# Performance work log

Measured on AMD Instinct MI355X. Metric: run time of the kernel, lower is better.

Reference implementation:

```python
import jax, jax.numpy as jnp
import numpy as np

FORWARD_STEPS = 50
DT = 0.1
EPS = 1e-5
BATCH = 1_000_000


def setup_inputs() -> dict:
    key = jax.random.key(0)
    k1, k2, k3 = jax.random.split(key, 3)
    # physically plausible ranges: speed 0-20 m/s, relative speed -2..2 m/s, gap 5-45 m
    vi = 20.0 * jax.random.uniform(k1, (BATCH,), dtype=jnp.float32)
    delta_v = 4.0 * jax.random.uniform(k2, (BATCH,), dtype=jnp.float32) - 2.0
    delta_d = 5.0 + 40.0 * jax.random.uniform(k3, (BATCH,), dtype=jnp.float32)
    # learned scalar IDM parameters (initializer values from the layer)
    params = {
        'vf': jnp.float32(25.0),
        'A': jnp.float32(2.0),
        'b': jnp.float32(3.0),
        's0': jnp.float32(3.0),
        'T': jnp.float32(2.0),
    }
    return {'vi': vi, 'delta_v': delta_v, 'delta_d': delta_d, **params}


def reference(vi, delta_v, delta_d, vf, A, b, s0, T):
    inv_2sqrtAb = 1.0 / (2.0 * jnp.sqrt(A * b))

    def step(carry, _):
        v, dv = carry
        s_star = s0 + jnp.maximum(0.0, v * T + v * dv * inv_2sqrtAb)
        ahat = A * (1.0 - (v / vf) ** 4 - (s_star / (delta_d + EPS)) ** 2)
        v = v + ahat * DT
        dv = dv - ahat * DT
        return (v, dv), ahat

    _, preds = jax.lax.scan(step, (vi, delta_v), None, length=FORWARD_STEPS)
    # preds: (steps, batch) -> (batch, steps) to match tf.stack(axis=1)
    return jnp.transpose(preds)
```

## Files before the change

kernel.cpp:

```cpp
#include <hip/hip_runtime.h>


namespace {

constexpr int STEPS = 50;
constexpr int BLOCK = 256;
constexpr float DT  = 0.1f;
constexpr float EPS = 1e-5f;

__global__ __launch_bounds__(BLOCK) void idm_forward(
    const float* __restrict__ vi_in,
    const float* __restrict__ dv_in,
    const float* __restrict__ dd_in,
    const float* __restrict__ p_vf,
    const float* __restrict__ p_A,
    const float* __restrict__ p_b,
    const float* __restrict__ p_s0,
    const float* __restrict__ p_T,
    float* __restrict__ out,
    int n)
{
    __shared__ __align__(16) float lds[BLOCK * STEPS];

    const int tid  = threadIdx.x;
    const int base = blockIdx.x * BLOCK;
    const int i    = base + tid;

    const float vf = p_vf[0];
    const float A  = p_A[0];
    const float b  = p_b[0];
    const float s0 = p_s0[0];
    const float T  = p_T[0];
    const float inv2   = 1.0f / (2.0f * sqrtf(A * b));
    const float inv_vf = 1.0f / vf;

    float v = 0.0f, dv = 0.0f, inv_dd = 1.0f;
    if (i < n) {
        v      = vi_in[i];
        dv     = dv_in[i];
        inv_dd = 1.0f / (dd_in[i] + EPS);
    }

    float acc[STEPS];
#pragma unroll
    for (int t = 0; t < STEPS; ++t) {
        const float s_star = s0 + fmaxf(0.0f, fmaf(v * dv, inv2, v * T));
        const float q  = s_star * inv_dd;
        const float r  = v * inv_vf;
        const float r2 = r * r;
        const float r4 = r2 * r2;
        const float ahat = A * (1.0f - r4 - q * q);
        acc[t] = ahat;
        v  = fmaf(ahat,  DT, v);
        dv = fmaf(ahat, -DT, dv);
    }

#pragma unroll
    for (int t = 0; t < STEPS; t += 2) {
        *reinterpret_cast<float2*>(&lds[tid * STEPS + t]) =
            make_float2(acc[t], acc[t + 1]);
    }
    __syncthreads();

    const long long out_base = (long long)base * STEPS;
    const long long total    = (long long)n * STEPS;
    int chunk = BLOCK * STEPS;
    if (out_base + chunk > total) chunk = (int)(total - out_base);

    float4* __restrict__ outv      = reinterpret_cast<float4*>(out + out_base);
    const float4* __restrict__ ldv = reinterpret_cast<const float4*>(lds);
    const int nv = chunk >> 2;
    for (int m = tid; m < nv; m += BLOCK) {
        outv[m] = ldv[m];
    }
    for (int k = (nv << 2) + tid; k < chunk; k += BLOCK) {
        out[out_base + k] = lds[k];
    }
}

}

extern "C" void kernel_launch(void* const* d_in, const int* in_sizes, int n_in,
                              void* d_out, int out_size, void* d_ws, size_t ws_size,
                              hipStream_t stream) {
    const float* vi = (const float*)d_in[0];
    const float* dv = (const float*)d_in[1];
    const float* dd = (const float*)d_in[2];
    const float* vf = (const float*)d_in[3];
    const float* A  = (const float*)d_in[4];
    const float* b  = (const float*)d_in[5];
    const float* s0 = (const float*)d_in[6];
    const float* T  = (const float*)d_in[7];
    float* out = (float*)d_out;

    const int n    = in_sizes[0];
    const int grid = (n + BLOCK - 1) / BLOCK;
    idm_forward<<<grid, BLOCK, 0, stream>>>(vi, dv, dd, vf, A, b, s0, T, out, n);
}
```

Before: 217.6 us.

## Stage output transpose per wavefront group through double-buffered LDS with nontemporal stores

Shrinks the LDS staging buffer from the whole block to two 64-thread group buffers. Groups are written and drained in turn, ping-ponging between the buffers, and the drain uses nontemporal float4 stores. The smaller LDS footprint and the occupancy hint of 6 blocks per CU are meant to let more blocks stay resident, which should help hide the store-bound output write. The cost is three extra block-wide barriers and serialized group drains, and the math also gains one fused multiply-add.

```diff
diff --git a/kernel.cpp b/kernel.cpp
--- a/kernel.cpp
+++ b/kernel.cpp
@@ -3,12 +3,17 @@
 
 namespace {
 
-constexpr int STEPS = 50;
-constexpr int BLOCK = 256;
+constexpr int STEPS   = 50;
+constexpr int BLOCK   = 256;
+constexpr int GROUP   = 64;
+constexpr int NGROUPS = BLOCK / GROUP;
 constexpr float DT  = 0.1f;
 constexpr float EPS = 1e-5f;
 
-__global__ __launch_bounds__(BLOCK) void idm_forward(
+typedef float f32x4 __attribute__((ext_vector_type(4)));
+typedef float f32x2 __attribute__((ext_vector_type(2)));
+
+__global__ __launch_bounds__(BLOCK, 6) void idm_forward(
     const float* __restrict__ vi_in,
     const float* __restrict__ dv_in,
     const float* __restrict__ dd_in,
@@ -20,7 +25,7 @@
     float* __restrict__ out,
     int n)
 {
-    __shared__ __align__(16) float lds[BLOCK * STEPS];
+    __shared__ __align__(16) float lds[2][GROUP * STEPS];
 
     const int tid  = threadIdx.x;
     const int base = blockIdx.x * BLOCK;
@@ -49,32 +54,54 @@
         const float r  = v * inv_vf;
         const float r2 = r * r;
         const float r4 = r2 * r2;
-        const float ahat = A * (1.0f - r4 - q * q);
+        const float ahat = A * fmaf(-q, q, 1.0f - r4);
         acc[t] = ahat;
         v  = fmaf(ahat,  DT, v);
         dv = fmaf(ahat, -DT, dv);
     }
 
+    const int g_of = tid >> 6;
+    const int l_of = tid & 63;
+
+    if (g_of == 0) {
 #pragma unroll
-    for (int t = 0; t < STEPS; t += 2) {
-        *reinterpret_cast<float2*>(&lds[tid * STEPS + t]) =
-            make_float2(acc[t], acc[t + 1]);
+        for (int t = 0; t < STEPS; t += 2) {
+            f32x2 w; w.x = acc[t]; w.y = acc[t + 1];
+            *reinterpret_cast<f32x2*>(&lds[0][l_of * STEPS + t]) = w;
+        }
     }
     __syncthreads();
 
-    const long long out_base = (long long)base * STEPS;
-    const long long total    = (long long)n * STEPS;
-    int chunk = BLOCK * STEPS;
-    if (out_base + chunk > total) chunk = (int)(total - out_base);
+    const long long total = (long long)n * STEPS;
 
-    float4* __restrict__ outv      = reinterpret_cast<float4*>(out + out_base);
-    const float4* __restrict__ ldv = reinterpret_cast<const float4*>(lds);
-    const int nv = chunk >> 2;
-    for (int m = tid; m < nv; m += BLOCK) {
-        outv[m] = ldv[m];
-    }
-    for (int k = (nv << 2) + tid; k < chunk; k += BLOCK) {
-        out[out_base + k] = lds[k];
+#pragma unroll
+    for (int g = 0; g < NGROUPS; ++g) {
+        if (g + 1 < NGROUPS && g_of == g + 1) {
+            const int nb = (g + 1) & 1;
+#pragma unroll
+            for (int t = 0; t < STEPS; t += 2) {
+                f32x2 w; w.x = acc[t]; w.y = acc[t + 1];
+                *reinterpret_cast<f32x2*>(&lds[nb][l_of * STEPS + t]) = w;
+            }
+        }
+
+        const long long gbase = (long long)(base + g * GROUP) * STEPS;
+        if (gbase < total) {
+            long long rem = total - gbase;
+            int chunk = GROUP * STEPS;
+            if (rem < chunk) chunk = (int)rem;
+            const int nv = chunk >> 2;
+            f32x4* __restrict__ outv      = reinterpret_cast<f32x4*>(out + gbase);
+            const f32x4* __restrict__ ldv =
+                reinterpret_cast<const f32x4*>(lds[g & 1]);
+            for (int m = tid; m < nv; m += BLOCK) {
+                __builtin_nontemporal_store(ldv[m], &outv[m]);
+            }
+            for (int k = (nv << 2) + tid; k < chunk; k += BLOCK) {
+                out[gbase + k] = lds[g & 1][k];
+            }
+        }
+        __syncthreads();
     }
 }
 
```

After: 228.0 us. +4.8%, slower.

## Stage output per wavefront in two half-waves to halve LDS and drop block barrier

Applied to the files above, without the earlier changes.

Output staging changes from one block-wide LDS buffer with a __syncthreads to a per-wavefront buffer holding 32 rows. Each half of the wave writes its 50 results in turn, and the whole wave then streams that half out with vector stores. LDS per block is halved, more blocks fit per CU (launch bounds now request 5), and the block barrier is gone, so the write-heavy kernel should overlap its stores better. It also folds the q*q term into an fma. Correctness depends on LDS ops within one wavefront staying in program order, since there is no barrier between reuse of the halves.

```diff
diff --git a/kernel.cpp b/kernel.cpp
--- a/kernel.cpp
+++ b/kernel.cpp
@@ -5,10 +5,14 @@
 
 constexpr int STEPS = 50;
 constexpr int BLOCK = 256;
+constexpr int HALF  = 32;
 constexpr float DT  = 0.1f;
 constexpr float EPS = 1e-5f;
 
-__global__ __launch_bounds__(BLOCK) void idm_forward(
+typedef float f32x4 __attribute__((ext_vector_type(4)));
+typedef float f32x2 __attribute__((ext_vector_type(2)));
+
+__global__ __launch_bounds__(BLOCK, 5) void idm_forward(
     const float* __restrict__ vi_in,
     const float* __restrict__ dv_in,
     const float* __restrict__ dd_in,
@@ -20,11 +24,12 @@
     float* __restrict__ out,
     int n)
 {
-    __shared__ __align__(16) float lds[BLOCK * STEPS];
+    __shared__ __align__(16) float lds[BLOCK / 64][HALF * STEPS];
 
     const int tid  = threadIdx.x;
-    const int base = blockIdx.x * BLOCK;
-    const int i    = base + tid;
+    const int wid  = tid >> 6;
+    const int lane = tid & 63;
+    const int i    = blockIdx.x * BLOCK + tid;
 
     const float vf = p_vf[0];
     const float A  = p_A[0];
@@ -49,32 +54,42 @@
         const float r  = v * inv_vf;
         const float r2 = r * r;
         const float r4 = r2 * r2;
-        const float ahat = A * (1.0f - r4 - q * q);
+        const float ahat = A * fmaf(-q, q, 1.0f - r4);
         acc[t] = ahat;
         v  = fmaf(ahat,  DT, v);
         dv = fmaf(ahat, -DT, dv);
     }
 
+    float* wbuf = lds[wid];
+    const long long total = (long long)n * STEPS;
+    const long long ebase = (long long)blockIdx.x * BLOCK + (wid << 6);
+
 #pragma unroll
-    for (int t = 0; t < STEPS; t += 2) {
-        *reinterpret_cast<float2*>(&lds[tid * STEPS + t]) =
-            make_float2(acc[t], acc[t + 1]);
-    }
-    __syncthreads();
+    for (int h = 0; h < 2; ++h) {
+        if ((lane >> 5) == h) {
+            const int l = lane & 31;
+#pragma unroll
+            for (int t = 0; t < STEPS; t += 2) {
+                f32x2 w; w.x = acc[t]; w.y = acc[t + 1];
+                *reinterpret_cast<f32x2*>(&wbuf[l * STEPS + t]) = w;
+            }
+        }
 
-    const long long out_base = (long long)base * STEPS;
-    const long long total    = (long long)n * STEPS;
-    int chunk = BLOCK * STEPS;
-    if (out_base + chunk > total) chunk = (int)(total - out_base);
-
-    float4* __restrict__ outv      = reinterpret_cast<float4*>(out + out_base);
-    const float4* __restrict__ ldv = reinterpret_cast<const float4*>(lds);
-    const int nv = chunk >> 2;
-    for (int m = tid; m < nv; m += BLOCK) {
-        outv[m] = ldv[m];
-    }
-    for (int k = (nv << 2) + tid; k < chunk; k += BLOCK) {
-        out[out_base + k] = lds[k];
+        const long long gbase = (ebase + h * HALF) * STEPS;
+        if (gbase < total) {
+            long long rem = total - gbase;
+            int chunk = HALF * STEPS;
+            if (rem < chunk) chunk = (int)rem;
+            const int nv = chunk >> 2;
+            f32x4* __restrict__ outv      = reinterpret_cast<f32x4*>(out + gbase);
+            const f32x4* __restrict__ ldv = reinterpret_cast<const f32x4*>(wbuf);
+            for (int m = lane; m < nv; m += 64) {
+                outv[m] = ldv[m];
+            }
+            for (int k = (nv << 2) + lane; k < chunk; k += 64) {
+                out[gbase + k] = wbuf[k];
+            }
+        }
     }
 }
 
```

Measured after the change: 218.0 us. Within noise of the previous version (+0.2%).
